# Performance work log

Measured on AMD Instinct MI355X. Metric: run time of the kernel, lower is better.

## Reference

```python
import jax, jax.numpy as jnp
import numpy as np

SLOPE = 25.0   # fast_sigmoid surrogate slope
BETA = 0.9     # LIF decay
THR = 1.0      # snntorch default threshold
STEPS = 10


@jax.custom_vjp
def spike(x):
    # Heaviside forward, fast-sigmoid surrogate backward
    return (x > 0).astype(x.dtype)

def _spike_fwd(x):
    return spike(x), x

def _spike_bwd(x, g):
    return (g / (SLOPE * jnp.abs(x) + 1.0) ** 2,)

spike.defvjp(_spike_fwd, _spike_bwd)


def lif(inp, mem):
    # snntorch Leaky, reset_mechanism='subtract': reset based on previous mem, detached
    reset = jax.lax.stop_gradient((mem > THR).astype(mem.dtype))
    mem = BETA * mem + inp - reset * THR
    spk = spike(mem - THR)
    return spk, mem


def setup_inputs() -> dict:
    key = jax.random.key(0)
    ks = jax.random.split(key, 4)
    B, IN, H, O = 65536, 512, 1024, 1
    x = jax.random.normal(ks[0], (B, IN), dtype=jnp.float32)
    W1 = jax.random.normal(ks[1], (IN, H), dtype=jnp.float32) / np.sqrt(IN)
    b1 = jnp.zeros((H,), jnp.float32)
    W2 = jax.random.normal(ks[2], (H, H), dtype=jnp.float32) / np.sqrt(H)
    b2 = jnp.zeros((H,), jnp.float32)
    Wo = jax.random.normal(ks[3], (H, O), dtype=jnp.float32) / np.sqrt(H)
    bo = jnp.zeros((O,), jnp.float32)
    return {"x": x, "W1": W1, "b1": b1, "W2": W2, "b2": b2, "Wo": Wo, "bo": bo}


def reference(x, W1, b1, W2, b2, Wo, bo):
    # fc1(x) is identical every timestep (x is static input current)
    cur1 = x @ W1 + b1                      # [B, H]
    B = x.shape[0]
    H = W1.shape[1]
    O = Wo.shape[1]
    m1 = jnp.zeros((B, H), x.dtype)
    m2 = jnp.zeros((B, H), x.dtype)
    mo = jnp.zeros((B, O), x.dtype)

    def step(carry, _):
        m1, m2, mo = carry
        s1, m1 = lif(cur1, m1)
        s2, m2 = lif(s1 @ W2 + b2, m2)
        _, mo = lif(s2 @ Wo + bo, mo)
        return (m1, m2, mo), mo

    _, recs = jax.lax.scan(step, (m1, m2, mo), None, length=STEPS)  # [STEPS, B, O]
    return recs.mean(0)
```

## Files before the change

kernel.cpp:

```cpp
#include <hip/hip_runtime.h>
#include <cstdint>
#include <cstddef>


typedef _Float16 f16;
typedef _Float16 f16x8 __attribute__((ext_vector_type(8)));
typedef float f32x4 __attribute__((ext_vector_type(4)));
typedef int i32x4 __attribute__((ext_vector_type(4)));

#define MFMA16(A, B, C) __builtin_amdgcn_mfma_f32_16x16x32_f16(A, B, C, 0, 0, 0)

static constexpr int BSZ = 65536;
static constexpr int IN = 512;
static constexpr int H = 1024;

__global__ void prep_dekker(const float* __restrict__ src, f16* __restrict__ dst) {
    int idx = blockIdx.x * 256 + threadIdx.x;
    int k = idx >> 10;
    int j = idx & 1023;
    float w = src[(size_t)k * 1024 + j];
    f16 hi = (f16)w;
    float lo = (w - (float)hi) * 2048.0f;
    size_t o = (size_t)j * 1024 + k;
    dst[o] = hi;
    dst[o + (size_t)H * H] = (f16)lo;
}

__global__ __launch_bounds__(256, 2) void k1_chain(
    const float* __restrict__ x, const float* __restrict__ w1,
    const float* __restrict__ b1, unsigned short* __restrict__ s1b) {
    __shared__ float xs[32][65];
    __shared__ float ws[32][256];
    const int hblk = blockIdx.x;
    const int bblk = blockIdx.y;
    const int tid = threadIdx.x;
    const int ht = tid & 15, bt = tid >> 4;
    const int h0 = hblk * 256, b0 = bblk * 64;

    float acc[4][16] = {};

    for (int kc = 0; kc < 512; kc += 32) {
        float4 xv[2], wv[8];
#pragma unroll
        for (int i = 0; i < 2; ++i) {
            int idx = tid + 256 * i;
            int br = idx >> 3, ks = idx & 7;
            xv[i] = *(const float4*)&x[(size_t)(b0 + br) * IN + kc + ks * 4];
        }
#pragma unroll
        for (int i = 0; i < 8; ++i) {
            int idx = tid + 256 * i;
            int kr = idx >> 6, c4 = idx & 63;
            wv[i] = *(const float4*)&w1[(size_t)(kc + kr) * H + h0 + c4 * 4];
        }
        __syncthreads();
#pragma unroll
        for (int i = 0; i < 2; ++i) {
            int idx = tid + 256 * i;
            int br = idx >> 3, ks = idx & 7;
            xs[ks * 4 + 0][br] = xv[i].x;
            xs[ks * 4 + 1][br] = xv[i].y;
            xs[ks * 4 + 2][br] = xv[i].z;
            xs[ks * 4 + 3][br] = xv[i].w;
        }
#pragma unroll
        for (int i = 0; i < 8; ++i) {
            int idx = tid + 256 * i;
            int kr = idx >> 6, c4 = idx & 63;
            *(float4*)&ws[kr][c4 * 4] = wv[i];
        }
        __syncthreads();
#pragma unroll
        for (int k = 0; k < 32; ++k) {
            float xr[4];
#pragma unroll
            for (int i = 0; i < 4; ++i) xr[i] = xs[k][bt * 4 + i];
            float wr[16];
#pragma unroll
            for (int g = 0; g < 4; ++g) {
                float4 t = *(const float4*)&ws[k][ht * 16 + g * 4];
                wr[g * 4 + 0] = t.x; wr[g * 4 + 1] = t.y;
                wr[g * 4 + 2] = t.z; wr[g * 4 + 3] = t.w;
            }
#pragma unroll
            for (int i = 0; i < 4; ++i)
#pragma unroll
                for (int j = 0; j < 16; ++j)
                    acc[i][j] = fmaf(xr[i], wr[j], acc[i][j]);
        }
    }

    float b1v[16];
#pragma unroll
    for (int j = 0; j < 16; ++j) b1v[j] = b1[h0 + ht * 16 + j];
#pragma unroll
    for (int i = 0; i < 4; ++i) {
        unsigned short outb[16];
#pragma unroll
        for (int j = 0; j < 16; ++j) {
            float c = __fadd_rn(acc[i][j], b1v[j]);
            float m = 0.0f;
            unsigned bits = 0u;
#pragma unroll
            for (int t = 0; t < 10; ++t) {
                float rst = (m > 1.0f) ? 1.0f : 0.0f;
                m = __fmul_rn(0.9f, m);
                m = __fadd_rn(m, c);
                m = __fsub_rn(m, rst);
                if (m > 1.0f) bits |= (1u << t);
            }
            outb[j] = (unsigned short)bits;
        }
        size_t off = (size_t)(b0 + bt * 4 + i) * H + h0 + ht * 16;
        *(int4*)&s1b[off] = ((const int4*)outb)[0];
        *(int4*)&s1b[off + 8] = ((const int4*)outb)[1];
    }
}

__global__ __launch_bounds__(256, 2) void k2_spikes_gemm(
    const unsigned short* __restrict__ s1bits, const f16* __restrict__ w2d,
    const float* __restrict__ b2, const float* __restrict__ wo,
    float* __restrict__ po) {
    __shared__ f16 Bs[2][2][32][40];
    const int jblk = blockIdx.x, bblk = blockIdx.y;
    const int tid = threadIdx.x;
    const int lane = tid & 63, wave = tid >> 6;
    const int l15 = lane & 15, loct = lane >> 4;
    const int sp = tid >> 7, sj = (tid >> 2) & 31, ss = tid & 3;

    const f16* bsrc = w2d + (size_t)sp * H * H + (size_t)(jblk * 32 + sj) * 1024 + ss * 8;
    const unsigned short* asrc =
        s1bits + (size_t)(bblk * 64 + wave * 16 + l15) * 1024 + loct * 8;

    f32x4 acc[10][2][2] = {};

    f16x8 gb = *(const f16x8*)bsrc;
    i32x4 ga = *(const i32x4*)asrc;
    int buf = 0;
    for (int kc = 0; kc < 1024; kc += 32) {
        *(f16x8*)&Bs[buf][sp][sj][ss * 8] = gb;
        int kn = (kc + 32 < 1024) ? (kc + 32) : 0;
        f16x8 gbn = *(const f16x8*)(bsrc + kn);
        i32x4 gan = *(const i32x4*)(asrc + kn);
        __syncthreads();
        f16x8 bf[2][2];
#pragma unroll
        for (int p = 0; p < 2; ++p)
#pragma unroll
            for (int cf = 0; cf < 2; ++cf)
                bf[p][cf] = *(const f16x8*)&Bs[buf][p][cf * 16 + l15][loct * 8];
#pragma unroll
        for (int t = 0; t < 10; ++t) {
            union { i32x4 i; f16x8 h; } u;
#pragma unroll
            for (int q = 0; q < 4; ++q)
                u.i[q] = (int)((((unsigned)ga[q] >> t) & 0x00010001u) * 0x3C00u);
            acc[t][0][0] = MFMA16(u.h, bf[0][0], acc[t][0][0]);
            acc[t][0][1] = MFMA16(u.h, bf[0][1], acc[t][0][1]);
            acc[t][1][0] = MFMA16(u.h, bf[1][0], acc[t][1][0]);
            acc[t][1][1] = MFMA16(u.h, bf[1][1], acc[t][1][1]);
        }
        gb = gbn; ga = gan;
        buf ^= 1;
    }

    int col0 = jblk * 32 + l15;
    float b2v0 = b2[col0], b2v1 = b2[col0 + 16];
    double wov0 = (double)wo[col0], wov1 = (double)wo[col0 + 16];
    int rowb = bblk * 64 + wave * 16 + loct * 4;
    float m2a[4] = {0.0f, 0.0f, 0.0f, 0.0f};
    float m2b[4] = {0.0f, 0.0f, 0.0f, 0.0f};
#pragma unroll
    for (int t = 0; t < 10; ++t) {
#pragma unroll
        for (int r = 0; r < 4; ++r) {
            float i0 = (float)((double)acc[t][0][0][r] + (double)acc[t][1][0][r] * 4.8828125e-4);
            i0 = __fadd_rn(i0, b2v0);
            float rst0 = (m2a[r] > 1.0f) ? 1.0f : 0.0f;
            m2a[r] = __fmul_rn(0.9f, m2a[r]);
            m2a[r] = __fadd_rn(m2a[r], i0);
            m2a[r] = __fsub_rn(m2a[r], rst0);
            float i1 = (float)((double)acc[t][0][1][r] + (double)acc[t][1][1][r] * 4.8828125e-4);
            i1 = __fadd_rn(i1, b2v1);
            float rst1 = (m2b[r] > 1.0f) ? 1.0f : 0.0f;
            m2b[r] = __fmul_rn(0.9f, m2b[r]);
            m2b[r] = __fadd_rn(m2b[r], i1);
            m2b[r] = __fsub_rn(m2b[r], rst1);
            double pv = ((m2a[r] > 1.0f) ? wov0 : 0.0) + ((m2b[r] > 1.0f) ? wov1 : 0.0);
            pv += __shfl_xor(pv, 1);
            pv += __shfl_xor(pv, 2);
            pv += __shfl_xor(pv, 4);
            pv += __shfl_xor(pv, 8);
            if (l15 == r)
                po[(size_t)(t * 32 + jblk) * BSZ + rowb + r] = (float)pv;
        }
    }
}

__global__ void k3_out(const float* __restrict__ po, const float* __restrict__ bo,
                       float* __restrict__ out) {
    int b = blockIdx.x * 256 + threadIdx.x;
    float mo = 0.0f, s = 0.0f;
    float bov = bo[0];
    for (int t = 0; t < 10; ++t) {
        float inp = 0.0f;
#pragma unroll
        for (int jb = 0; jb < 32; ++jb) inp += po[(size_t)(t * 32 + jb) * BSZ + b];
        inp = __fadd_rn(inp, bov);
        float rst = (mo > 1.0f) ? 1.0f : 0.0f;
        mo = __fmul_rn(0.9f, mo);
        mo = __fadd_rn(mo, inp);
        mo = __fsub_rn(mo, rst);
        s += mo;
    }
    out[b] = s / 10.0f;
}

extern "C" void kernel_launch(void* const* d_in, const int* in_sizes, int n_in,
                              void* d_out, int out_size, void* d_ws, size_t ws_size,
                              hipStream_t stream) {
    (void)in_sizes; (void)n_in; (void)out_size; (void)ws_size;
    const float* x  = (const float*)d_in[0];
    const float* W1 = (const float*)d_in[1];
    const float* b1 = (const float*)d_in[2];
    const float* W2 = (const float*)d_in[3];
    const float* b2 = (const float*)d_in[4];
    const float* Wo = (const float*)d_in[5];
    const float* bo = (const float*)d_in[6];
    float* out = (float*)d_out;

    char* ws = (char*)d_ws;
    f16* w2d = (f16*)ws;
    unsigned short* s1bits = (unsigned short*)(ws + ((size_t)16 << 20));
    float* po = (float*)(ws + ((size_t)160 << 20));

    prep_dekker<<<dim3((H * H) / 256), 256, 0, stream>>>(W2, w2d);
    k1_chain<<<dim3(4, BSZ / 64), 256, 0, stream>>>(x, W1, b1, s1bits);
    k2_spikes_gemm<<<dim3(H / 32, BSZ / 64), 256, 0, stream>>>(s1bits, w2d, b2, Wo, po);
    k3_out<<<dim3(BSZ / 256), 256, 0, stream>>>(po, bo, out);
}
```

Measured before the change: 3.582 ms.

## Split spike-GEMM timesteps across two wave halves with LDS-staged spike bits

Grows the spike GEMM block to 512 threads. Each half of the waves now accumulates five of the ten timesteps, which halves the accumulator registers per thread and allows higher occupancy. Spike bits are staged through LDS alongside the weights, and the bit-to-f16 expansion uses a single shift-and-mask with rescaled combine factors. The second half picks up the membrane state from the first through shared memory, which adds a barrier and serialises the LIF epilogue between the halves.

```diff
diff --git a/kernel.cpp b/kernel.cpp
--- a/kernel.cpp
+++ b/kernel.cpp
@@ -117,32 +117,40 @@
     }
 }
 
-__global__ __launch_bounds__(256, 2) void k2_spikes_gemm(
+__global__ __launch_bounds__(512, 4) void k2_spikes_gemm(
     const unsigned short* __restrict__ s1bits, const f16* __restrict__ w2d,
     const float* __restrict__ b2, const float* __restrict__ wo,
     float* __restrict__ po) {
+    __shared__ unsigned short As[2][64][40];
     __shared__ f16 Bs[2][2][32][40];
+    __shared__ float m2x[4][64][8];
     const int jblk = blockIdx.x, bblk = blockIdx.y;
     const int tid = threadIdx.x;
     const int lane = tid & 63, wave = tid >> 6;
+    const int strip = wave & 3, thalf = wave >> 2;
     const int l15 = lane & 15, loct = lane >> 4;
-    const int sp = tid >> 7, sj = (tid >> 2) & 31, ss = tid & 3;
-
-    const f16* bsrc = w2d + (size_t)sp * H * H + (size_t)(jblk * 32 + sj) * 1024 + ss * 8;
-    const unsigned short* asrc =
-        s1bits + (size_t)(bblk * 64 + wave * 16 + l15) * 1024 + loct * 8;
-
-    f32x4 acc[10][2][2] = {};
-
-    f16x8 gb = *(const f16x8*)bsrc;
-    i32x4 ga = *(const i32x4*)asrc;
+    const int t0 = thalf * 5;
+
+    const bool stageB = (tid >= 256);
+    const int s = tid & 255;
+    const int arow = s >> 2, aseg = s & 3;
+    const int bpl = s >> 7, brow = (s >> 2) & 31, bseg = s & 3;
+
+    const unsigned short* ag = s1bits + (size_t)(bblk * 64 + arow) * 1024 + aseg * 8;
+    const f16* bg = w2d + (size_t)bpl * H * H + (size_t)(jblk * 32 + brow) * 1024 + bseg * 8;
+
+    f32x4 acc[5][2][2] = {};
+
+    i32x4 gv = stageB ? *(const i32x4*)bg : *(const i32x4*)ag;
+
     int buf = 0;
     for (int kc = 0; kc < 1024; kc += 32) {
-        *(f16x8*)&Bs[buf][sp][sj][ss * 8] = gb;
-        int kn = (kc + 32 < 1024) ? (kc + 32) : 0;
-        f16x8 gbn = *(const f16x8*)(bsrc + kn);
-        i32x4 gan = *(const i32x4*)(asrc + kn);
+        if (stageB) *(i32x4*)&Bs[buf][bpl][brow][bseg * 8] = gv;
+        else        *(i32x4*)&As[buf][arow][aseg * 8] = gv;
+        int kn = (kc + 32) & 1023;
+        i32x4 gn = stageB ? *(const i32x4*)(bg + kn) : *(const i32x4*)(ag + kn);
         __syncthreads();
+        i32x4 am = *(const i32x4*)&As[buf][strip * 16 + l15][loct * 8];
         f16x8 bf[2][2];
 #pragma unroll
         for (int p = 0; p < 2; ++p)
@@ -150,49 +158,91 @@
             for (int cf = 0; cf < 2; ++cf)
                 bf[p][cf] = *(const f16x8*)&Bs[buf][p][cf * 16 + l15][loct * 8];
 #pragma unroll
-        for (int t = 0; t < 10; ++t) {
+        for (int tt = 0; tt < 5; ++tt) {
+            const int sh = 10 - (t0 + tt);
             union { i32x4 i; f16x8 h; } u;
 #pragma unroll
             for (int q = 0; q < 4; ++q)
-                u.i[q] = (int)((((unsigned)ga[q] >> t) & 0x00010001u) * 0x3C00u);
-            acc[t][0][0] = MFMA16(u.h, bf[0][0], acc[t][0][0]);
-            acc[t][0][1] = MFMA16(u.h, bf[0][1], acc[t][0][1]);
-            acc[t][1][0] = MFMA16(u.h, bf[1][0], acc[t][1][0]);
-            acc[t][1][1] = MFMA16(u.h, bf[1][1], acc[t][1][1]);
-        }
-        gb = gbn; ga = gan;
+                u.i[q] = (int)(((unsigned)am[q] << sh) & 0x04000400u);
+            acc[tt][0][0] = MFMA16(u.h, bf[0][0], acc[tt][0][0]);
+            acc[tt][0][1] = MFMA16(u.h, bf[0][1], acc[tt][0][1]);
+            acc[tt][1][0] = MFMA16(u.h, bf[1][0], acc[tt][1][0]);
+            acc[tt][1][1] = MFMA16(u.h, bf[1][1], acc[tt][1][1]);
+        }
+        gv = gn;
         buf ^= 1;
     }
 
     int col0 = jblk * 32 + l15;
     float b2v0 = b2[col0], b2v1 = b2[col0 + 16];
     double wov0 = (double)wo[col0], wov1 = (double)wo[col0 + 16];
-    int rowb = bblk * 64 + wave * 16 + loct * 4;
+    int rowb = bblk * 64 + strip * 16 + loct * 4;
     float m2a[4] = {0.0f, 0.0f, 0.0f, 0.0f};
     float m2b[4] = {0.0f, 0.0f, 0.0f, 0.0f};
-#pragma unroll
-    for (int t = 0; t < 10; ++t) {
+
+    if (thalf == 0) {
+#pragma unroll
+        for (int tt = 0; tt < 5; ++tt) {
+#pragma unroll
+            for (int r = 0; r < 4; ++r) {
+                float i0 = (float)((double)acc[tt][0][0][r] * 16384.0 + (double)acc[tt][1][0][r] * 8.0);
+                i0 = __fadd_rn(i0, b2v0);
+                float rst0 = (m2a[r] > 1.0f) ? 1.0f : 0.0f;
+                m2a[r] = __fmul_rn(0.9f, m2a[r]);
+                m2a[r] = __fadd_rn(m2a[r], i0);
+                m2a[r] = __fsub_rn(m2a[r], rst0);
+                float i1 = (float)((double)acc[tt][0][1][r] * 16384.0 + (double)acc[tt][1][1][r] * 8.0);
+                i1 = __fadd_rn(i1, b2v1);
+                float rst1 = (m2b[r] > 1.0f) ? 1.0f : 0.0f;
+                m2b[r] = __fmul_rn(0.9f, m2b[r]);
+                m2b[r] = __fadd_rn(m2b[r], i1);
+                m2b[r] = __fsub_rn(m2b[r], rst1);
+                double pv = ((m2a[r] > 1.0f) ? wov0 : 0.0) + ((m2b[r] > 1.0f) ? wov1 : 0.0);
+                pv += __shfl_xor(pv, 1);
+                pv += __shfl_xor(pv, 2);
+                pv += __shfl_xor(pv, 4);
+                pv += __shfl_xor(pv, 8);
+                if (l15 == r)
+                    po[(size_t)(tt * 32 + jblk) * BSZ + rowb + r] = (float)pv;
+            }
+        }
 #pragma unroll
         for (int r = 0; r < 4; ++r) {
-            float i0 = (float)((double)acc[t][0][0][r] + (double)acc[t][1][0][r] * 4.8828125e-4);
-            i0 = __fadd_rn(i0, b2v0);
-            float rst0 = (m2a[r] > 1.0f) ? 1.0f : 0.0f;
-            m2a[r] = __fmul_rn(0.9f, m2a[r]);
-            m2a[r] = __fadd_rn(m2a[r], i0);
-            m2a[r] = __fsub_rn(m2a[r], rst0);
-            float i1 = (float)((double)acc[t][0][1][r] + (double)acc[t][1][1][r] * 4.8828125e-4);
-            i1 = __fadd_rn(i1, b2v1);
-            float rst1 = (m2b[r] > 1.0f) ? 1.0f : 0.0f;
-            m2b[r] = __fmul_rn(0.9f, m2b[r]);
-            m2b[r] = __fadd_rn(m2b[r], i1);
-            m2b[r] = __fsub_rn(m2b[r], rst1);
-            double pv = ((m2a[r] > 1.0f) ? wov0 : 0.0) + ((m2b[r] > 1.0f) ? wov1 : 0.0);
-            pv += __shfl_xor(pv, 1);
-            pv += __shfl_xor(pv, 2);
-            pv += __shfl_xor(pv, 4);
-            pv += __shfl_xor(pv, 8);
-            if (l15 == r)
-                po[(size_t)(t * 32 + jblk) * BSZ + rowb + r] = (float)pv;
+            m2x[strip][lane][r] = m2a[r];
+            m2x[strip][lane][4 + r] = m2b[r];
+        }
+    }
+    __syncthreads();
+    if (thalf == 1) {
+#pragma unroll
+        for (int r = 0; r < 4; ++r) {
+            m2a[r] = m2x[strip][lane][r];
+            m2b[r] = m2x[strip][lane][4 + r];
+        }
+#pragma unroll
+        for (int tt = 0; tt < 5; ++tt) {
+#pragma unroll
+            for (int r = 0; r < 4; ++r) {
+                float i0 = (float)((double)acc[tt][0][0][r] * 16384.0 + (double)acc[tt][1][0][r] * 8.0);
+                i0 = __fadd_rn(i0, b2v0);
+                float rst0 = (m2a[r] > 1.0f) ? 1.0f : 0.0f;
+                m2a[r] = __fmul_rn(0.9f, m2a[r]);
+                m2a[r] = __fadd_rn(m2a[r], i0);
+                m2a[r] = __fsub_rn(m2a[r], rst0);
+                float i1 = (float)((double)acc[tt][0][1][r] * 16384.0 + (double)acc[tt][1][1][r] * 8.0);
+                i1 = __fadd_rn(i1, b2v1);
+                float rst1 = (m2b[r] > 1.0f) ? 1.0f : 0.0f;
+                m2b[r] = __fmul_rn(0.9f, m2b[r]);
+                m2b[r] = __fadd_rn(m2b[r], i1);
+                m2b[r] = __fsub_rn(m2b[r], rst1);
+                double pv = ((m2a[r] > 1.0f) ? wov0 : 0.0) + ((m2b[r] > 1.0f) ? wov1 : 0.0);
+                pv += __shfl_xor(pv, 1);
+                pv += __shfl_xor(pv, 2);
+                pv += __shfl_xor(pv, 4);
+                pv += __shfl_xor(pv, 8);
+                if (l15 == r)
+                    po[(size_t)((5 + tt) * 32 + jblk) * BSZ + rowb + r] = (float)pv;
+            }
         }
     }
 }
@@ -236,6 +286,6 @@
 
     prep_dekker<<<dim3((H * H) / 256), 256, 0, stream>>>(W2, w2d);
     k1_chain<<<dim3(4, BSZ / 64), 256, 0, stream>>>(x, W1, b1, s1bits);
-    k2_spikes_gemm<<<dim3(H / 32, BSZ / 64), 256, 0, stream>>>(s1bits, w2d, b2, Wo, po);
+    k2_spikes_gemm<<<dim3(H / 32, BSZ / 64), 512, 0, stream>>>(s1bits, w2d, b2, Wo, po);
     k3_out<<<dim3(BSZ / 256), 256, 0, stream>>>(po, bo, out);
 }
```

Measured after the change: 3.622 ms. About the same (+1.1%).
